# Kernel tuning notes

Measured on AMD Instinct MI355X. Metric: run time of the kernel, lower is better.

The kernel has to match this reference:

```python
import jax, jax.numpy as jnp
import numpy as np

B, S, L, D = 128, 256, 200, 768
POS_VOCAB, POS_DIM = 60, 50
REDUC, HID, TAGS, POL = 400, 150, 5, 4


def setup_inputs() -> dict:
    key = jax.random.key(0)
    ks = jax.random.split(key, 12)
    bert_vectors = jax.random.normal(ks[0], (B, S, D), dtype=jnp.float32)
    # ragged subword spans: word j covers subwords [start_j, end_j] (inclusive), length 1..3,
    # skipping the [CLS] token at index 0. Clipped to S-1 (long sentences just truncate).
    rng = np.random.default_rng(0)
    lens = rng.integers(1, 4, size=(B, L))
    cum = np.cumsum(lens, axis=1)
    starts = 1 + cum - lens
    ends = cum
    starts = np.minimum(starts, S - 1)
    ends = np.minimum(ends, S - 1)
    ends = np.maximum(ends, starts)
    positions = jnp.asarray(np.stack([starts, ends], axis=-1), dtype=jnp.int32)
    postag = jax.random.randint(ks[1], (B, L), 1, POS_VOCAB).astype(jnp.int32)

    def lin(k, o, i):
        return jax.random.normal(k, (o, i), jnp.float32) / np.float32(np.sqrt(i))

    return dict(
        bert_vectors=bert_vectors,
        positions=positions,
        postag=postag,
        embed_table=jax.random.normal(ks[2], (POS_VOCAB, POS_DIM), jnp.float32) * 0.02,
        W_reduc=lin(ks[3], REDUC, D + POS_DIM), b_reduc=jnp.zeros((REDUC,), jnp.float32),
        W_ap=lin(ks[4], HID, REDUC), b_ap=jnp.zeros((HID,), jnp.float32),
        W_op=lin(ks[5], HID, REDUC), b_op=jnp.zeros((HID,), jnp.float32),
        W_ap2=lin(ks[6], HID, REDUC), b_ap2=jnp.zeros((HID,), jnp.float32),
        W_op2=lin(ks[7], HID, REDUC), b_op2=jnp.zeros((HID,), jnp.float32),
        W_aptag=lin(ks[8], TAGS, HID), b_aptag=jnp.zeros((TAGS,), jnp.float32),
        W_optag=lin(ks[9], TAGS, HID), b_optag=jnp.zeros((TAGS,), jnp.float32),
        W_bi=lin(ks[10], POL * HID, HID + 1),
    )


def _pool_subwords(vectors, positions):
    # variable-length mean pooling of subword vectors into word vectors
    # vectors: [B,S,D], positions: [B,L,2] -> [B,L,D]
    idx = jnp.arange(S)[None, None, :]                      # [1,1,S]
    p0 = positions[..., 0][..., None]                       # [B,L,1]
    p1 = positions[..., 1][..., None]
    m = ((idx >= p0) & (idx <= p1)).astype(vectors.dtype)   # [B,L,S]
    cnt = jnp.maximum(m.sum(-1, keepdims=True), 1.0)
    return jnp.einsum('bls,bsd->bld', m, vectors) / cnt


def reference(bert_vectors, positions, postag, embed_table,
              W_reduc, b_reduc, W_ap, b_ap, W_op, b_op,
              W_ap2, b_ap2, W_op2, b_op2,
              W_aptag, b_aptag, W_optag, b_optag, W_bi):
    word_vecs = _pool_subwords(bert_vectors, positions)                 # [B,L,D]
    pos_emb = embed_table[postag]                                       # [B,L,50]
    h = jnp.concatenate([pos_emb, word_vecs], axis=-1)                  # [B,L,D+50]
    reduc = jnp.einsum('blf,of->blo', h, W_reduc) + b_reduc             # [B,L,400]
    ap_rep = jax.nn.relu(jnp.einsum('blf,of->blo', reduc, W_ap) + b_ap)
    op_rep = jax.nn.relu(jnp.einsum('blf,of->blo', reduc, W_op) + b_op)
    ap_node = jax.nn.relu(jnp.einsum('blf,of->blo', reduc, W_ap2) + b_ap2)
    op_node = jax.nn.relu(jnp.einsum('blf,of->blo', reduc, W_op2) + b_op2)
    ap_out = jnp.einsum('blf,of->blo', ap_rep, W_aptag) + b_aptag       # [B,L,5]
    op_out = jnp.einsum('blf,of->blo', op_rep, W_optag) + b_optag       # [B,L,5]
    # Biaffine(150,150,POL,bias=(True,False))
    ones = jnp.ones((B, L, 1), ap_node.dtype)
    in1 = jnp.concatenate([ap_node, ones], axis=-1)                     # [B,L,151]
    affine = jnp.einsum('bli,oi->blo', in1, W_bi).reshape(B, L * POL, HID)
    tri = jnp.einsum('bkh,bmh->bkm', affine, op_node)                   # [B,L*POL,L]
    triplet_out = tri.transpose(0, 2, 1).reshape(B, L, L, POL)          # [B,L2,L1,POL]
    return (ap_out, op_out, triplet_out)
```

## Files before the change

kernel.cpp:

```cpp
#include <hip/hip_runtime.h>
#include <hip/hip_bf16.h>

#define Bsz 128
#define Ssz 256
#define Lsz 200
#define Dsz 768
#define POS_DIM 50
#define TAGS 5
#define NROW 25600
#define FIN 818
#define KH 832
#define KR 416
#define KD 160

typedef __attribute__((ext_vector_type(8))) short short8;
typedef __attribute__((ext_vector_type(4))) short short4v;
typedef __attribute__((ext_vector_type(4))) float floatx4;

__device__ __forceinline__ short f2bf(float v) {
    __hip_bfloat16 h = __float2bfloat16(v);
    short s; __builtin_memcpy(&s, &h, 2); return s;
}
__device__ __forceinline__ float bf2f(short s) {
    __hip_bfloat16 h; __builtin_memcpy(&h, &s, 2);
    return __bfloat162float(h);
}

__device__ __forceinline__ void gload16(const short* g, short* l) {
    __builtin_amdgcn_global_load_lds(
        (const __attribute__((address_space(1))) void*)g,
        (__attribute__((address_space(3))) void*)l, 16, 0, 0);
}

__global__ void prep_kernel(const float* __restrict__ W_reduc,
                            const float* __restrict__ W_ap, const float* __restrict__ W_op,
                            const float* __restrict__ W_ap2, const float* __restrict__ W_op2,
                            const float* __restrict__ W_bi,
                            const float* __restrict__ b_reduc,
                            const float* __restrict__ b_ap, const float* __restrict__ b_op,
                            const float* __restrict__ b_ap2, const float* __restrict__ b_op2,
                            short* __restrict__ Wr_bf, short* __restrict__ Wh_bf,
                            short* __restrict__ Wbi_bf,
                            float* __restrict__ br_pad, float* __restrict__ bh_pad,
                            float* __restrict__ bbi_pad)
{
    int i = blockIdx.x * blockDim.x + threadIdx.x;
    if (i < 512 * KH) {
        int r = i / KH, k = i % KH;
        float v = 0.0f;
        if (r < 400) {
            if (k < 768)       v = W_reduc[r * FIN + POS_DIM + k];
            else if (k < 818)  v = W_reduc[r * FIN + (k - 768)];
        }
        Wr_bf[i] = f2bf(v);
    }
    if (i < 640 * KR) {
        int r = i / KR, c = i % KR;
        float v = 0.0f;
        if (r < 600 && c < 400) {
            const float* src = (r < 150) ? W_ap : (r < 300) ? W_op : (r < 450) ? W_ap2 : W_op2;
            v = src[(r % 150) * 400 + c];
        }
        Wh_bf[i] = f2bf(v);
    }
    if (i < 640 * KD) {
        int r = i / KD, c = i % KD;
        Wbi_bf[i] = (r < 600 && c < 150) ? f2bf(W_bi[r * 151 + c]) : (short)0;
    }
    if (i < KR) br_pad[i] = (i < 400) ? b_reduc[i] : 0.0f;
    if (i < 640) {
        float v = 0.0f;
        if (i < 600) {
            const float* bs = (i < 150) ? b_ap : (i < 300) ? b_op : (i < 450) ? b_ap2 : b_op2;
            v = bs[i % 150];
        }
        bh_pad[i] = v;
        bbi_pad[i] = (i < 600) ? W_bi[i * 151 + 150] : 0.0f;
    }
}

__global__ __launch_bounds__(256) void pool_kernel(
    const float* __restrict__ bert,
    const int* __restrict__ positions,
    const int* __restrict__ postag,
    const float* __restrict__ embed,
    short* __restrict__ h_bf)
{
    int row = blockIdx.x;
    int b = row / Lsz;
    int st = positions[row * 2 + 0];
    int en = positions[row * 2 + 1];
    int tag = postag[row];
    int span = en - st + 1;
    float inv = 1.0f / (float)span;
    const float* base = bert + ((long)b * Ssz + st) * Dsz;
    short* hr = h_bf + (long)row * KH;

    int t = threadIdx.x;
    int c0 = t * 4;
    if (c0 >= KH) return;
    short4v o;
    if (c0 < 768) {
        float4 s = {0.f, 0.f, 0.f, 0.f};
        for (int i = 0; i < span; ++i) {
            float4 v = *(const float4*)(base + i * Dsz + c0);
            s.x += v.x; s.y += v.y; s.z += v.z; s.w += v.w;
        }
        o.x = f2bf(s.x * inv); o.y = f2bf(s.y * inv);
        o.z = f2bf(s.z * inv); o.w = f2bf(s.w * inv);
    } else {
        const float* e = embed + tag * POS_DIM;
#pragma unroll
        for (int j = 0; j < 4; ++j) {
            int c = c0 + j - 768;
            float v = (c < POS_DIM) ? e[c] : 0.0f;
            ((short*)&o)[j] = f2bf(v);
        }
    }
    *(short4v*)(hr + c0) = o;
}

__global__ __launch_bounds__(256) void gemm_mfma(
    const short* __restrict__ A, long long sAb, int lda,
    const short* __restrict__ Bt, long long sBb, int ldb,
    const float* __restrict__ bias,
    short* __restrict__ outB, float* __restrict__ outF, long long sCb, int ldc,
    int M, int Nv, int K, int mode)
{
    __shared__ __align__(16) short AB[16384];

    int bz = blockIdx.z;
    A += (long long)bz * sAb;
    Bt += (long long)bz * sBb;

    int row0 = blockIdx.y * 128;
    int col0 = blockIdx.x * 128;
    int tid = threadIdx.x;
    int lane = tid & 63;
    int wv = tid >> 6;
    int lm = lane & 15, lk = lane >> 4;
    int wr = (wv >> 1) * 64;
    int wc = (wv & 1) * 64;

    int c0 = tid, c1 = tid + 256;
    const short* gA0 = A + (long)(row0 + (c0 & 127)) * lda + (c0 >> 7) * 8;
    const short* gA1 = A + (long)(row0 + (c1 & 127)) * lda + (c1 >> 7) * 8;
    const short* gB0 = Bt + (long)(col0 + (c0 & 127)) * ldb + (c0 >> 7) * 8;
    const short* gB1 = Bt + (long)(col0 + (c1 & 127)) * ldb + (c1 >> 7) * 8;

    floatx4 acc[4][4];
#pragma unroll
    for (int i = 0; i < 4; ++i)
#pragma unroll
        for (int j = 0; j < 4; ++j)
            acc[i][j] = (floatx4){0.f, 0.f, 0.f, 0.f};

    auto stage = [&](int buf, int koff) {
        short* base = &AB[buf * 8192];
        gload16(gA0 + koff, base + c0 * 8);
        gload16(gA1 + koff, base + c1 * 8);
        gload16(gB0 + koff, base + 4096 + c0 * 8);
        gload16(gB1 + koff, base + 4096 + c1 * 8);
    };
    auto compute = [&](int buf) {
        const short* fa = &AB[buf * 8192 + (lk * 128 + wr + lm) * 8];
        const short* fb = &AB[buf * 8192 + 4096 + (lk * 128 + wc + lm) * 8];
        short8 a[4], b[4];
#pragma unroll
        for (int mt = 0; mt < 4; ++mt) a[mt] = *(const short8*)(fa + mt * 128);
#pragma unroll
        for (int nt = 0; nt < 4; ++nt) b[nt] = *(const short8*)(fb + nt * 128);
#pragma unroll
        for (int mt = 0; mt < 4; ++mt)
#pragma unroll
            for (int nt = 0; nt < 4; ++nt)
                acc[mt][nt] = __builtin_amdgcn_mfma_f32_16x16x32_bf16(
                    a[mt], b[nt], acc[mt][nt], 0, 0, 0);
    };

    int nt = K >> 5;
    stage(0, 0);
    __syncthreads();
    int cur = 0;
    for (int t = 0; t + 1 < nt; ++t) {
        stage(cur ^ 1, (t + 1) << 5);
        compute(cur);
        __syncthreads();
        cur ^= 1;
    }
    compute(cur);

#pragma unroll
    for (int mt = 0; mt < 4; ++mt) {
#pragma unroll
        for (int nt = 0; nt < 4; ++nt) {
#pragma unroll
            for (int r = 0; r < 4; ++r) {
                int gm = row0 + wr + mt * 16 + lk * 4 + r;
                int gn = col0 + wc + nt * 16 + lm;
                float v = acc[mt][nt][r];
                if (mode == 0) {
                    if (gn < Nv)
                        outB[(long)gm * ldc + gn] = f2bf(v + bias[gn]);
                } else if (mode == 1) {
                    if (gn < 600) {
                        v = fmaxf(v + bias[gn], 0.0f);
                        outB[((long)(gn / 150) * NROW + gm) * KD + gn % 150] = f2bf(v);
                    } else if (gn < 640) {
                        int q = gn - 600;
                        outB[((long)(q / 10) * NROW + gm) * KD + 150 + q % 10] = 0;
                    }
                } else if (mode == 2) {
                    int bb = gm / 200, l = gm % 200;
                    if (gn < 600) {
                        v += bias[gn];
                        outB[((long)bb * 800 + l * 4 + gn / 150) * KD + gn % 150] = f2bf(v);
                    } else if (gn < 640) {
                        int q = gn - 600;
                        outB[((long)bb * 800 + l * 4 + q / 10) * KD + 150 + q % 10] = 0;
                    }
                } else {
                    if (gm < M && gn < Nv)
                        outF[(long long)bz * sCb + (long)gm * ldc + gn] = v;
                }
            }
        }
    }
}

__global__ __launch_bounds__(256) void tags_kernel(
    const short* __restrict__ hid4,
    const float* __restrict__ W_aptag, const float* __restrict__ b_aptag,
    const float* __restrict__ W_optag, const float* __restrict__ b_optag,
    float* __restrict__ out_ap, float* __restrict__ out_op)
{
    int wave = threadIdx.x / 64;
    int lane = threadIdx.x % 64;
    int row = blockIdx.x * 4 + wave;
    if (row >= NROW) return;

#pragma unroll
    for (int which = 0; which < 2; ++which) {
        const short* rep = hid4 + ((long)which * NROW + row) * KD;
        const float* W = which ? W_optag : W_aptag;
        const float* bb = which ? b_optag : b_aptag;
        float* out = which ? out_op : out_ap;
        float v0 = bf2f(rep[lane]);
        float v1 = bf2f(rep[64 + lane]);
        float v2 = (lane < 22) ? bf2f(rep[128 + lane]) : 0.0f;
#pragma unroll
        for (int t = 0; t < TAGS; ++t) {
            const float* w = W + t * 150;
            float p = v0 * w[lane] + v1 * w[64 + lane] +
                      ((lane < 22) ? v2 * w[128 + lane] : 0.0f);
#pragma unroll
            for (int off = 32; off > 0; off >>= 1) p += __shfl_down(p, off);
            if (lane == 0) out[row * TAGS + t] = p + bb[t];
        }
    }
}

extern "C" void kernel_launch(void* const* d_in, const int* in_sizes, int n_in,
                              void* d_out, int out_size, void* d_ws, size_t ws_size,
                              hipStream_t stream)
{
    const float* bert      = (const float*)d_in[0];
    const int*   positions = (const int*)d_in[1];
    const int*   postag    = (const int*)d_in[2];
    const float* embed     = (const float*)d_in[3];
    const float* W_reduc   = (const float*)d_in[4];
    const float* b_reduc   = (const float*)d_in[5];
    const float* W_ap      = (const float*)d_in[6];
    const float* b_ap      = (const float*)d_in[7];
    const float* W_op      = (const float*)d_in[8];
    const float* b_op      = (const float*)d_in[9];
    const float* W_ap2     = (const float*)d_in[10];
    const float* b_ap2     = (const float*)d_in[11];
    const float* W_op2     = (const float*)d_in[12];
    const float* b_op2     = (const float*)d_in[13];
    const float* W_aptag   = (const float*)d_in[14];
    const float* b_aptag   = (const float*)d_in[15];
    const float* W_optag   = (const float*)d_in[16];
    const float* b_optag   = (const float*)d_in[17];
    const float* W_bi      = (const float*)d_in[18];

    float* out = (float*)d_out;
    float* out_ap  = out;
    float* out_op  = out + NROW * TAGS;
    float* out_tri = out + 2 * NROW * TAGS;

    short* ws = (short*)d_ws;
    short* h_bf     = ws;
    short* affine   = h_bf;
    short* reduc_bf = h_bf + (long)NROW * KH;
    short* hid4     = reduc_bf + (long)NROW * KR;
    short* Wr_bf    = hid4 + (long)4 * NROW * KD;
    short* Wh_bf    = Wr_bf + 512 * KH;
    short* Wbi_bf   = Wh_bf + 640 * KR;
    float* br_pad   = (float*)(Wbi_bf + 640 * KD);
    float* bh_pad   = br_pad + KR;
    float* bbi_pad  = bh_pad + 640;

    prep_kernel<<<(512 * KH + 255) / 256, 256, 0, stream>>>(
        W_reduc, W_ap, W_op, W_ap2, W_op2, W_bi,
        b_reduc, b_ap, b_op, b_ap2, b_op2,
        Wr_bf, Wh_bf, Wbi_bf, br_pad, bh_pad, bbi_pad);

    pool_kernel<<<NROW, 256, 0, stream>>>(bert, positions, postag, embed, h_bf);

    {
        dim3 g(4, NROW / 128, 1);
        gemm_mfma<<<g, 256, 0, stream>>>(h_bf, 0, KH, Wr_bf, 0, KH, br_pad,
                                         reduc_bf, nullptr, 0, KR,
                                         NROW, KR, KH, 0);
    }
    {
        dim3 g(5, NROW / 128, 1);
        gemm_mfma<<<g, 256, 0, stream>>>(reduc_bf, 0, KR, Wh_bf, 0, KR, bh_pad,
                                         hid4, nullptr, 0, 0,
                                         NROW, 600, KR, 1);
    }
    tags_kernel<<<NROW / 4, 256, 0, stream>>>(hid4, W_aptag, b_aptag,
                                              W_optag, b_optag, out_ap, out_op);
    {
        dim3 g(5, NROW / 128, 1);
        gemm_mfma<<<g, 256, 0, stream>>>(hid4 + (long)2 * NROW * KD, 0, KD,
                                         Wbi_bf, 0, KD, bbi_pad,
                                         affine, nullptr, 0, 0,
                                         NROW, 600, KD, 2);
    }
    {
        dim3 g(7, 2, Bsz);
        gemm_mfma<<<g, 256, 0, stream>>>(hid4 + (long)3 * NROW * KD, (long long)200 * KD, KD,
                                         affine, (long long)800 * KD, KD, nullptr,
                                         nullptr, out_tri, (long long)200 * 800, 800,
                                         200, 800, KD, 3);
    }
}
```

Measured before the change: 478.8 us.

## Fold reduction linear into hidden projections and swizzle GEMM blocks across XCDs

```diff
diff --git a/kernel.cpp b/kernel.cpp
--- a/kernel.cpp
+++ b/kernel.cpp
@@ -10,7 +10,6 @@
 #define NROW 25600
 #define FIN 818
 #define KH 832
-#define KR 416
 #define KD 160
 
 typedef __attribute__((ext_vector_type(8))) short short8;
@@ -32,50 +31,74 @@
         (__attribute__((address_space(3))) void*)l, 16, 0, 0);
 }
 
-__global__ void prep_kernel(const float* __restrict__ W_reduc,
-                            const float* __restrict__ W_ap, const float* __restrict__ W_op,
+__global__ void prep_kernel(const float* __restrict__ W_ap, const float* __restrict__ W_op,
                             const float* __restrict__ W_ap2, const float* __restrict__ W_op2,
                             const float* __restrict__ W_bi,
                             const float* __restrict__ b_reduc,
                             const float* __restrict__ b_ap, const float* __restrict__ b_op,
                             const float* __restrict__ b_ap2, const float* __restrict__ b_op2,
-                            short* __restrict__ Wr_bf, short* __restrict__ Wh_bf,
                             short* __restrict__ Wbi_bf,
-                            float* __restrict__ br_pad, float* __restrict__ bh_pad,
-                            float* __restrict__ bbi_pad)
+                            float* __restrict__ b2, float* __restrict__ bbi_pad)
 {
     int i = blockIdx.x * blockDim.x + threadIdx.x;
-    if (i < 512 * KH) {
-        int r = i / KH, k = i % KH;
-        float v = 0.0f;
-        if (r < 400) {
-            if (k < 768)       v = W_reduc[r * FIN + POS_DIM + k];
-            else if (k < 818)  v = W_reduc[r * FIN + (k - 768)];
-        }
-        Wr_bf[i] = f2bf(v);
-    }
-    if (i < 640 * KR) {
-        int r = i / KR, c = i % KR;
-        float v = 0.0f;
-        if (r < 600 && c < 400) {
-            const float* src = (r < 150) ? W_ap : (r < 300) ? W_op : (r < 450) ? W_ap2 : W_op2;
-            v = src[(r % 150) * 400 + c];
-        }
-        Wh_bf[i] = f2bf(v);
-    }
     if (i < 640 * KD) {
         int r = i / KD, c = i % KD;
         Wbi_bf[i] = (r < 600 && c < 150) ? f2bf(W_bi[r * 151 + c]) : (short)0;
     }
-    if (i < KR) br_pad[i] = (i < 400) ? b_reduc[i] : 0.0f;
     if (i < 640) {
         float v = 0.0f;
         if (i < 600) {
             const float* bs = (i < 150) ? b_ap : (i < 300) ? b_op : (i < 450) ? b_ap2 : b_op2;
             v = bs[i % 150];
-        }
-        bh_pad[i] = v;
+            const float* wsrc = (i < 150) ? W_ap : (i < 300) ? W_op : (i < 450) ? W_ap2 : W_op2;
+            const float* wrow = wsrc + (i % 150) * 400;
+            float d = 0.0f;
+            for (int c = 0; c < 400; ++c) d += wrow[c] * b_reduc[c];
+            v += d;
+        }
+        b2[i] = v;
         bbi_pad[i] = (i < 600) ? W_bi[i * 151 + 150] : 0.0f;
+    }
+}
+
+__global__ __launch_bounds__(256) void fold_kernel(
+    const float* __restrict__ W_ap, const float* __restrict__ W_op,
+    const float* __restrict__ W_ap2, const float* __restrict__ W_op2,
+    const float* __restrict__ W_reduc,
+    short* __restrict__ W2_bf)
+{
+    __shared__ float whs[8][400];
+    int r0 = blockIdx.x * 8;
+    for (int idx = threadIdx.x; idx < 8 * 400; idx += 256) {
+        int rr = idx / 400, c = idx % 400;
+        int r = r0 + rr;
+        float v = 0.0f;
+        if (r < 600) {
+            const float* src = (r < 150) ? W_ap : (r < 300) ? W_op : (r < 450) ? W_ap2 : W_op2;
+            v = src[(r % 150) * 400 + c];
+        }
+        whs[rr][c] = v;
+    }
+    __syncthreads();
+#pragma unroll
+    for (int j = 0; j < 4; ++j) {
+        int k = threadIdx.x + j * 256;
+        if (k >= KH) break;
+        int sc = 0; bool valid = true;
+        if (k < 768)      sc = POS_DIM + k;
+        else if (k < 818) sc = k - 768;
+        else              valid = false;
+        float acc[8] = {0, 0, 0, 0, 0, 0, 0, 0};
+        if (valid) {
+            for (int c = 0; c < 400; ++c) {
+                float v = W_reduc[c * FIN + sc];
+#pragma unroll
+                for (int rr = 0; rr < 8; ++rr) acc[rr] += whs[rr][c] * v;
+            }
+        }
+#pragma unroll
+        for (int rr = 0; rr < 8; ++rr)
+            W2_bf[(long)(r0 + rr) * KH + k] = f2bf(acc[rr]);
     }
 }
 
@@ -133,8 +156,19 @@
     A += (long long)bz * sAb;
     Bt += (long long)bz * sBb;
 
-    int row0 = blockIdx.y * 128;
-    int col0 = blockIdx.x * 128;
+    int bx = blockIdx.x, by = blockIdx.y;
+    if (gridDim.z == 1) {
+        int nwg = gridDim.x * gridDim.y;
+        int orig = by * gridDim.x + bx;
+        int q = nwg >> 3, r = nwg & 7;
+        int xcd = orig & 7, idx = orig >> 3;
+        int swz = (xcd < r ? xcd * (q + 1) : r * (q + 1) + (xcd - r) * q) + idx;
+        bx = swz % gridDim.x;
+        by = swz / gridDim.x;
+    }
+
+    int row0 = by * 128;
+    int col0 = bx * 128;
     int tid = threadIdx.x;
     int lane = tid & 63;
     int wv = tid >> 6;
@@ -292,33 +326,26 @@
     short* ws = (short*)d_ws;
     short* h_bf     = ws;
     short* affine   = h_bf;
-    short* reduc_bf = h_bf + (long)NROW * KH;
-    short* hid4     = reduc_bf + (long)NROW * KR;
-    short* Wr_bf    = hid4 + (long)4 * NROW * KD;
-    short* Wh_bf    = Wr_bf + 512 * KH;
-    short* Wbi_bf   = Wh_bf + 640 * KR;
-    float* br_pad   = (float*)(Wbi_bf + 640 * KD);
-    float* bh_pad   = br_pad + KR;
-    float* bbi_pad  = bh_pad + 640;
-
-    prep_kernel<<<(512 * KH + 255) / 256, 256, 0, stream>>>(
-        W_reduc, W_ap, W_op, W_ap2, W_op2, W_bi,
+    short* hid4     = h_bf + (long)NROW * KH;
+    short* W2_bf    = hid4 + (long)4 * NROW * KD;
+    short* Wbi_bf   = W2_bf + 640 * KH;
+    float* b2       = (float*)(Wbi_bf + 640 * KD);
+    float* bbi_pad  = b2 + 640;
+
+    prep_kernel<<<(640 * KD + 255) / 256, 256, 0, stream>>>(
+        W_ap, W_op, W_ap2, W_op2, W_bi,
         b_reduc, b_ap, b_op, b_ap2, b_op2,
-        Wr_bf, Wh_bf, Wbi_bf, br_pad, bh_pad, bbi_pad);
+        Wbi_bf, b2, bbi_pad);
+
+    fold_kernel<<<80, 256, 0, stream>>>(W_ap, W_op, W_ap2, W_op2, W_reduc, W2_bf);
 
     pool_kernel<<<NROW, 256, 0, stream>>>(bert, positions, postag, embed, h_bf);
 
-    {
-        dim3 g(4, NROW / 128, 1);
-        gemm_mfma<<<g, 256, 0, stream>>>(h_bf, 0, KH, Wr_bf, 0, KH, br_pad,
-                                         reduc_bf, nullptr, 0, KR,
-                                         NROW, KR, KH, 0);
-    }
     {
         dim3 g(5, NROW / 128, 1);
-        gemm_mfma<<<g, 256, 0, stream>>>(reduc_bf, 0, KR, Wh_bf, 0, KR, bh_pad,
+        gemm_mfma<<<g, 256, 0, stream>>>(h_bf, 0, KH, W2_bf, 0, KH, b2,
                                          hid4, nullptr, 0, 0,
-                                         NROW, 600, KR, 1);
+                                         NROW, 600, KH, 1);
     }
     tags_kernel<<<NROW / 4, 256, 0, stream>>>(hid4, W_aptag, b_aptag,
                                               W_optag, b_optag, out_ap, out_op);
```

Result: slower. 589.9 us (+23.2%).
